# Kernel optimization log

Hardware: AMD Instinct MI355X
Metric: run time of the kernel (lower is better)

The kernel has to match this reference:

```python
import jax, jax.numpy as jnp
import numpy as np

EMB_DIM = 512
NUM_HEADS = 8
SEQ_LEN = 4096
BATCH = 4


def setup_inputs() -> dict:
    key = jax.random.key(0)
    k = jax.random.split(key, 5)
    E = EMB_DIM
    scale = 1.0 / np.sqrt(E)
    x = jax.random.normal(k[0], (BATCH, SEQ_LEN, E), dtype=jnp.float32)
    Wqkv = jax.random.normal(k[1], (E, 3 * E), dtype=jnp.float32) * scale
    bqkv = jax.random.normal(k[2], (3 * E,), dtype=jnp.float32) * 0.01
    Wo = jax.random.normal(k[3], (E, E), dtype=jnp.float32) * scale
    bo = jax.random.normal(k[4], (E,), dtype=jnp.float32) * 0.01
    return {"x": x, "Wqkv": Wqkv, "bqkv": bqkv, "Wo": Wo, "bo": bo}


def reference(x, Wqkv, bqkv, Wo, bo):
    B, S, E = x.shape
    H = NUM_HEADS
    Dh = E // H
    qkv = x @ Wqkv + bqkv                      # [B,S,3E]
    q, k, v = jnp.split(qkv, 3, axis=-1)
    # [B,S,E] -> [B,H,S,Dh]
    q = q.reshape(B, S, H, Dh).transpose(0, 2, 1, 3)
    k = k.reshape(B, S, H, Dh).transpose(0, 2, 1, 3)
    v = v.reshape(B, S, H, Dh).transpose(0, 2, 1, 3)
    att = jnp.einsum("bhsd,bhtd->bhst", q, k) / jnp.sqrt(jnp.asarray(Dh, x.dtype))
    causal = jnp.tril(jnp.ones((S, S), dtype=bool))
    att = jnp.where(causal[None, None], att, -jnp.inf)
    att = jax.nn.softmax(att, axis=-1)
    out = jnp.einsum("bhst,bhtd->bhsd", att, v)  # [B,H,S,Dh]
    out = out.transpose(0, 2, 1, 3).reshape(B, S, E)
    return out @ Wo + bo
```

## Files before the change

kernel.cpp:

```cpp
#include <hip/hip_runtime.h>
#include <math.h>

#define NB 4
#define NS 4096
#define NE 512
#define NH 8
#define ND 64
#define N3 1536
#define NM (NB*NS)

typedef __attribute__((ext_vector_type(8))) short bf16x8;
typedef __attribute__((ext_vector_type(4))) float f32x4;
typedef unsigned short ushort_t;

#define QSCALE 0.18033688011f

extern "C" __device__ float __ocml_native_exp2_f32(float);

__device__ __forceinline__ unsigned int pk2bf(float a, float b) {
    unsigned int r;
    asm("v_cvt_pk_bf16_f32 %0, %1, %2" : "=v"(r) : "v"(a), "v"(b));
    return r;
}

__device__ __forceinline__ unsigned short f2bf(float f) {
    return (unsigned short)(pk2bf(f, f) & 0xFFFFu);
}

typedef __attribute__((address_space(1))) const void g_void;
typedef __attribute__((address_space(3))) void l_void;
__device__ __forceinline__ void cp16(const void* g, void* l) {
    __builtin_amdgcn_global_load_lds((g_void*)g, (l_void*)l, 16, 0, 0);
}

__global__ __launch_bounds__(256)
void cast_x(const float* __restrict__ x, ushort_t* __restrict__ xb) {
    const size_t i = ((size_t)blockIdx.x * 256 + threadIdx.x) * 4;
    float4 v = *(const float4*)&x[i];
    uint2 o;
    o.x = pk2bf(v.x, v.y);
    o.y = pk2bf(v.z, v.w);
    *(uint2*)&xb[i] = o;
}

__global__ __launch_bounds__(256)
void cast_wT(const float* __restrict__ W, ushort_t* __restrict__ WT, int N) {
    __shared__ ushort_t T[64][72];
    const int t = threadIdx.x;
    const int k0 = blockIdx.y * 64, n0 = blockIdx.x * 64;
    const int tx = t & 15, ty = t >> 4;
    #pragma unroll
    for (int p = 0; p < 4; ++p) {
        const int r = p * 16 + ty;
        float4 v = *(const float4*)&W[(size_t)(k0 + r) * N + n0 + tx * 4];
        const unsigned int u01 = pk2bf(v.x, v.y);
        const unsigned int u23 = pk2bf(v.z, v.w);
        T[tx*4+0][r] = (ushort_t)(u01 & 0xFFFFu);
        T[tx*4+1][r] = (ushort_t)(u01 >> 16);
        T[tx*4+2][r] = (ushort_t)(u23 & 0xFFFFu);
        T[tx*4+3][r] = (ushort_t)(u23 >> 16);
    }
    __syncthreads();
    const int nn = t >> 2, kc = (t & 3) * 16;
    uint4 a = *(uint4*)&T[nn][kc];
    uint4 b = *(uint4*)&T[nn][kc + 8];
    *(uint4*)&WT[(size_t)(n0 + nn) * 512 + k0 + kc]     = a;
    *(uint4*)&WT[(size_t)(n0 + nn) * 512 + k0 + kc + 8] = b;
}

__global__ __launch_bounds__(256)
void qkv_mfma(const ushort_t* __restrict__ xb, const ushort_t* __restrict__ WT,
              const float* __restrict__ bqkv,
              ushort_t* __restrict__ Qb, ushort_t* __restrict__ Kb,
              ushort_t* __restrict__ Vb)
{
    __shared__ ushort_t As[128 * 32];
    __shared__ ushort_t Bs[128 * 32];
    const int tid = threadIdx.x;
    const int lane = tid & 63, w = tid >> 6;
    const int col = lane & 15, quad = lane >> 4;
    const int wm = w & 1, wn = w >> 1;
    const int m0 = blockIdx.y * 128;
    const int nblk = blockIdx.x * 128;

    const int arow = tid >> 2, ach = (tid & 3) * 8;
    const ushort_t* aSrc = xb + (size_t)(m0 + arow) * 512 + ach;
    const ushort_t* bSrc = WT + (size_t)(nblk + arow) * 512 + ach;
    ushort_t* aDst = As + tid * 8;
    ushort_t* bDst = Bs + tid * 8;

    f32x4 acc[4][4];
    #pragma unroll
    for (int i = 0; i < 4; ++i)
        #pragma unroll
        for (int j = 0; j < 4; ++j)
            #pragma unroll
            for (int r = 0; r < 4; ++r) acc[i][j][r] = 0.f;

    for (int k0 = 0; k0 < 512; k0 += 32) {
        __syncthreads();
        cp16(aSrc + k0, aDst);
        cp16(aSrc + 64 * 512 + k0, aDst + 2048);
        cp16(bSrc + k0, bDst);
        cp16(bSrc + 64 * 512 + k0, bDst + 2048);
        __syncthreads();
        bf16x8 af[4], bf[4];
        #pragma unroll
        for (int mt = 0; mt < 4; ++mt)
            af[mt] = *(const bf16x8*)&As[(wm*64 + mt*16 + col) * 32 + quad*8];
        #pragma unroll
        for (int nt = 0; nt < 4; ++nt)
            bf[nt] = *(const bf16x8*)&Bs[(wn*64 + nt*16 + col) * 32 + quad*8];
        #pragma unroll
        for (int nt = 0; nt < 4; ++nt)
            #pragma unroll
            for (int mt = 0; mt < 4; ++mt)
                acc[mt][nt] = __builtin_amdgcn_mfma_f32_16x16x32_bf16(
                    af[mt], bf[nt], acc[mt][nt], 0, 0, 0);
    }

    const int which = nblk >> 9;
    const float scale = (which == 0) ? QSCALE : 1.0f;
    const int b = m0 >> 12;
    const int s0 = m0 & (NS - 1);
    float bias[4];
    int hh[4], dd[4];
    #pragma unroll
    for (int nt = 0; nt < 4; ++nt) {
        const int n = nblk + wn*64 + nt*16 + col;
        bias[nt] = bqkv[n];
        const int e = n & (NE - 1);
        hh[nt] = e >> 6; dd[nt] = e & 63;
    }
    if (which == 2) {
        #pragma unroll
        for (int mt = 0; mt < 4; ++mt) {
            const int s = s0 + wm*64 + mt*16 + quad*4;
            #pragma unroll
            for (int nt = 0; nt < 4; ++nt) {
                uint2 pv;
                pv.x = pk2bf(acc[mt][nt][0] + bias[nt],
                             acc[mt][nt][1] + bias[nt]);
                pv.y = pk2bf(acc[mt][nt][2] + bias[nt],
                             acc[mt][nt][3] + bias[nt]);
                *(uint2*)&Vb[((size_t)(b*NH + hh[nt]) * ND + dd[nt]) * NS + s] = pv;
            }
        }
    } else {
        ushort_t* dst = (which == 0) ? Qb : Kb;
        #pragma unroll
        for (int mt = 0; mt < 4; ++mt) {
            const int s = s0 + wm*64 + mt*16 + quad*4;
            #pragma unroll
            for (int nt = 0; nt < 4; ++nt) {
                const unsigned int u01 =
                    pk2bf((acc[mt][nt][0] + bias[nt]) * scale,
                          (acc[mt][nt][1] + bias[nt]) * scale);
                const unsigned int u23 =
                    pk2bf((acc[mt][nt][2] + bias[nt]) * scale,
                          (acc[mt][nt][3] + bias[nt]) * scale);
                const size_t a0 = ((size_t)(b*NH + hh[nt]) * NS + s) * ND + dd[nt];
                dst[a0]          = (ushort_t)(u01 & 0xFFFFu);
                dst[a0 + ND]     = (ushort_t)(u01 >> 16);
                dst[a0 + 2*ND]   = (ushort_t)(u23 & 0xFFFFu);
                dst[a0 + 3*ND]   = (ushort_t)(u23 >> 16);
            }
        }
    }
}

__global__ __launch_bounds__(256)
void flash_mfma(const ushort_t* __restrict__ Qb,
                const ushort_t* __restrict__ Kb,
                const ushort_t* __restrict__ Vb,
                ushort_t* __restrict__ Ob)
{
    __shared__ __align__(16) ushort_t Ks[64][72];
    __shared__ __align__(16) ushort_t VT[64][72];
    __shared__ __align__(16) ushort_t Ps[4][32][72];

    const int tid  = threadIdx.x;
    const int w    = tid >> 6;
    const int lane = tid & 63;
    const int col  = lane & 15;
    const int quad = lane >> 4;
    const int qpair = blockIdx.x;
    const int bh   = blockIdx.y;
    const size_t base = (size_t)bh * NS * ND;

    const int r  = tid & 63;
    const int dg = tid >> 6;
    const ushort_t* kbase = Kb + base + (size_t)r * ND + dg*16;
    const ushort_t* vbase = Vb + base + (size_t)r * NS + dg*16;

    bf16x8 ones;
    {
        const short o = (col == 0) ? (short)0x3F80 : (short)0;
        #pragma unroll
        for (int j = 0; j < 8; ++j) ones[j] = o;
    }

    #pragma unroll 1
    for (int phase = 0; phase < 2; ++phase) {
        const int qv = phase ? (31 - qpair) : qpair;

        bf16x8 aq[2][2];
        #pragma unroll
        for (int mt = 0; mt < 2; ++mt)
            #pragma unroll
            for (int kh = 0; kh < 2; ++kh)
                aq[mt][kh] = *(const bf16x8*)
                    &Qb[base + (size_t)(qv*128 + w*32 + mt*16 + col) * ND
                        + kh*32 + quad*8];

        f32x4 acc[2][4];
        f32x4 lacc[2];
        #pragma unroll
        for (int mt = 0; mt < 2; ++mt) {
            #pragma unroll
            for (int r2 = 0; r2 < 4; ++r2) lacc[mt][r2] = 0.f;
            #pragma unroll
            for (int nt = 0; nt < 4; ++nt)
                #pragma unroll
                for (int r2 = 0; r2 < 4; ++r2) acc[mt][nt][r2] = 0.f;
        }

        const int nkt = 2 * qv + 2;

        uint4 kr0, kr1, vr0, vr1;
        {
            const ushort_t* ks = kbase;
            kr0 = *(const uint4*)ks;
            kr1 = *(const uint4*)(ks + 8);
            const ushort_t* vs = vbase;
            vr0 = *(const uint4*)vs;
            vr1 = *(const uint4*)(vs + 8);
        }

        for (int kt = 0; kt < nkt; ++kt) {
            __syncthreads();
            *(uint4*)&Ks[r][dg*16]     = kr0;
            *(uint4*)&Ks[r][dg*16 + 8] = kr1;
            *(uint4*)&VT[r][dg*16]     = vr0;
            *(uint4*)&VT[r][dg*16 + 8] = vr1;
            __syncthreads();

            if (kt + 1 < nkt) {
                const ushort_t* ks = kbase + (size_t)(kt+1) * 64 * ND;
                kr0 = *(const uint4*)ks;
                kr1 = *(const uint4*)(ks + 8);
                const ushort_t* vs = vbase + (kt+1) * 64;
                vr0 = *(const uint4*)vs;
                vr1 = *(const uint4*)(vs + 8);
            }

            if (kt*64 >= qv*128 + w*32 + 32) continue;

            f32x4 s[2][4];
            #pragma unroll
            for (int mt = 0; mt < 2; ++mt)
                #pragma unroll
                for (int nt = 0; nt < 4; ++nt)
                    #pragma unroll
                    for (int r2 = 0; r2 < 4; ++r2) s[mt][nt][r2] = 0.f;

            #pragma unroll
            for (int nt = 0; nt < 4; ++nt)
                #pragma unroll
                for (int kh = 0; kh < 2; ++kh) {
                    bf16x8 ak = *(const bf16x8*)&Ks[nt*16 + col][kh*32 + quad*8];
                    #pragma unroll
                    for (int mt = 0; mt < 2; ++mt)
                        s[mt][nt] = __builtin_amdgcn_mfma_f32_16x16x32_bf16(
                            ak, aq[mt][kh], s[mt][nt], 0, 0, 0);
                }

            if (kt >= 2 * qv) {
                #pragma unroll
                for (int mt = 0; mt < 2; ++mt) {
                    const int qrow = qv*128 + w*32 + mt*16 + col;
                    #pragma unroll
                    for (int nt = 0; nt < 4; ++nt) {
                        const int key = kt*64 + nt*16 + quad*4;
                        #pragma unroll
                        for (int reg = 0; reg < 4; ++reg)
                            if (key + reg > qrow) s[mt][nt][reg] = -1e30f;
                    }
                }
            }

            #pragma unroll
            for (int mt = 0; mt < 2; ++mt)
                #pragma unroll
                for (int nt = 0; nt < 4; ++nt) {
                    uint2 pw;
                    pw.x = pk2bf(__ocml_native_exp2_f32(s[mt][nt][0]),
                                 __ocml_native_exp2_f32(s[mt][nt][1]));
                    pw.y = pk2bf(__ocml_native_exp2_f32(s[mt][nt][2]),
                                 __ocml_native_exp2_f32(s[mt][nt][3]));
                    *(uint2*)&Ps[w][mt*16 + col][nt*16 + quad*4] = pw;
                }

            bf16x8 ap[2][2];
            #pragma unroll
            for (int mt = 0; mt < 2; ++mt)
                #pragma unroll
                for (int kh = 0; kh < 2; ++kh)
                    ap[mt][kh] = *(const bf16x8*)&Ps[w][mt*16 + col][kh*32 + quad*8];

            #pragma unroll
            for (int mt = 0; mt < 2; ++mt)
                #pragma unroll
                for (int kh = 0; kh < 2; ++kh)
                    lacc[mt] = __builtin_amdgcn_mfma_f32_16x16x32_bf16(
                        ap[mt][kh], ones, lacc[mt], 0, 0, 0);

            #pragma unroll
            for (int nt = 0; nt < 4; ++nt)
                #pragma unroll
                for (int kh = 0; kh < 2; ++kh) {
                    bf16x8 bv = *(const bf16x8*)&VT[nt*16 + col][kh*32 + quad*8];
                    #pragma unroll
                    for (int mt = 0; mt < 2; ++mt)
                        acc[mt][nt] = __builtin_amdgcn_mfma_f32_16x16x32_bf16(
                            ap[mt][kh], bv, acc[mt][nt], 0, 0, 0);
                }
        }

        #pragma unroll
        for (int mt = 0; mt < 2; ++mt)
            #pragma unroll
            for (int reg = 0; reg < 4; ++reg) {
                const float l = __shfl(lacc[mt][reg], lane & 48, 64);
                const float inv = 1.f / l;
                const int row = qv*128 + w*32 + mt*16 + quad*4 + reg;
                const unsigned int u01 = pk2bf(acc[0 + (mt<<0)][0][reg] * 0.f +
                                               acc[mt][0][reg] * inv,
                                               acc[mt][1][reg] * inv);
                const unsigned int u23 = pk2bf(acc[mt][2][reg] * inv,
                                               acc[mt][3][reg] * inv);
                ushort_t* op = &Ob[base + (size_t)row * ND + col];
                op[0]  = (ushort_t)(u01 & 0xFFFFu);
                op[16] = (ushort_t)(u01 >> 16);
                op[32] = (ushort_t)(u23 & 0xFFFFu);
                op[48] = (ushort_t)(u23 >> 16);
            }
    }
}

__global__ __launch_bounds__(256)
void out_mfma(const ushort_t* __restrict__ Ob, const ushort_t* __restrict__ WT,
              const float* __restrict__ bo, float* __restrict__ out)
{
    __shared__ ushort_t As[128 * 32];
    __shared__ ushort_t Bs[128 * 32];
    const int tid = threadIdx.x;
    const int lane = tid & 63, w = tid >> 6;
    const int col = lane & 15, quad = lane >> 4;
    const int wm = w & 1, wn = w >> 1;
    const int m0 = blockIdx.y * 128;
    const int nblk = blockIdx.x * 128;

    const int arow = tid >> 2, ach = (tid & 3) * 8;
    const int bblk = m0 >> 12;
    const int s0 = m0 & (NS - 1);
    const ushort_t* bSrc = WT + (size_t)(nblk + arow) * 512 + ach;
    ushort_t* aDst = As + tid * 8;
    ushort_t* bDst = Bs + tid * 8;

    f32x4 acc[4][4];
    #pragma unroll
    for (int i = 0; i < 4; ++i)
        #pragma unroll
        for (int j = 0; j < 4; ++j)
            #pragma unroll
            for (int r = 0; r < 4; ++r) acc[i][j][r] = 0.f;

    for (int k0 = 0; k0 < 512; k0 += 32) {
        __syncthreads();
        const int h = k0 >> 6, koff = k0 & 63;
        const ushort_t* aS =
            Ob + ((size_t)(bblk*NH + h) * NS + s0 + arow) * ND + koff + ach;
        cp16(aS, aDst);
        cp16(aS + 64 * ND, aDst + 2048);
        cp16(bSrc + k0, bDst);
        cp16(bSrc + 64 * 512 + k0, bDst + 2048);
        __syncthreads();
        bf16x8 af[4], bf[4];
        #pragma unroll
        for (int mt = 0; mt < 4; ++mt)
            af[mt] = *(const bf16x8*)&As[(wm*64 + mt*16 + col) * 32 + quad*8];
        #pragma unroll
        for (int nt = 0; nt < 4; ++nt)
            bf[nt] = *(const bf16x8*)&Bs[(wn*64 + nt*16 + col) * 32 + quad*8];
        #pragma unroll
        for (int nt = 0; nt < 4; ++nt)
            #pragma unroll
            for (int mt = 0; mt < 4; ++mt)
                acc[mt][nt] = __builtin_amdgcn_mfma_f32_16x16x32_bf16(
                    af[mt], bf[nt], acc[mt][nt], 0, 0, 0);
    }

    float bias[4];
    #pragma unroll
    for (int nt = 0; nt < 4; ++nt)
        bias[nt] = bo[nblk + wn*64 + nt*16 + col];
    #pragma unroll
    for (int mt = 0; mt < 4; ++mt)
        #pragma unroll
        for (int reg = 0; reg < 4; ++reg) {
            const int m = m0 + wm*64 + mt*16 + quad*4 + reg;
            #pragma unroll
            for (int nt = 0; nt < 4; ++nt)
                out[(size_t)m * NE + nblk + wn*64 + nt*16 + col] =
                    acc[mt][nt][reg] + bias[nt];
        }
}

extern "C" void kernel_launch(void* const* d_in, const int* in_sizes, int n_in,
                              void* d_out, int out_size, void* d_ws, size_t ws_size,
                              hipStream_t stream) {
    const float* x    = (const float*)d_in[0];
    const float* Wqkv = (const float*)d_in[1];
    const float* bqkv = (const float*)d_in[2];
    const float* Wo   = (const float*)d_in[3];
    const float* bo   = (const float*)d_in[4];
    float* out = (float*)d_out;

    const size_t per = (size_t)NB * NH * NS * ND;
    ushort_t* ws = (ushort_t*)d_ws;
    ushort_t* xb     = ws;
    ushort_t* Ob     = ws;
    ushort_t* Qb     = ws + per;
    ushort_t* Kb     = Qb + per;
    ushort_t* Vb     = Kb + per;
    ushort_t* WqkvT  = Vb + per;
    ushort_t* WoT    = WqkvT + (size_t)N3 * NE;

    dim3 blk(256);
    cast_x<<<dim3(NM * NE / 1024), blk, 0, stream>>>(x, xb);
    cast_wT<<<dim3(N3/64, NE/64), blk, 0, stream>>>(Wqkv, WqkvT, N3);
    cast_wT<<<dim3(NE/64, NE/64), blk, 0, stream>>>(Wo, WoT, NE);
    qkv_mfma<<<dim3(N3/128, NM/128), blk, 0, stream>>>(xb, WqkvT, bqkv, Qb, Kb, Vb);
    flash_mfma<<<dim3(16, NB*NH), blk, 0, stream>>>(Qb, Kb, Vb, Ob);
    out_mfma<<<dim3(NE/128, NM/128), blk, 0, stream>>>(Ob, WoT, bo, out);
}
```

Measured before the change: 256.7 us.

## Split flash attention block into 8 waves of 16 query rows each

The flash attention kernel now launches 512 threads per block with 8 waves, each owning 16 query rows instead of 32. The K/V tile staging is split across the 8 waves at 8 elements per thread, and each wave keeps its own P tile in shared memory. The aim is more waves per block to hide latency and finer causal skipping per wave. In exchange each wave does half the MFMA work per K/V tile load, so there is more synchronisation and LDS traffic per unit of compute.

```diff
diff --git a/kernel.cpp b/kernel.cpp
--- a/kernel.cpp
+++ b/kernel.cpp
@@ -169,7 +169,7 @@
     }
 }
 
-__global__ __launch_bounds__(256)
+__global__ __launch_bounds__(512)
 void flash_mfma(const ushort_t* __restrict__ Qb,
                 const ushort_t* __restrict__ Kb,
                 const ushort_t* __restrict__ Vb,
@@ -177,7 +177,7 @@
 {
     __shared__ __align__(16) ushort_t Ks[64][72];
     __shared__ __align__(16) ushort_t VT[64][72];
-    __shared__ __align__(16) ushort_t Ps[4][32][72];
+    __shared__ __align__(16) ushort_t Ps[8][16][72];
 
     const int tid  = threadIdx.x;
     const int w    = tid >> 6;
@@ -190,8 +190,8 @@
 
     const int r  = tid & 63;
     const int dg = tid >> 6;
-    const ushort_t* kbase = Kb + base + (size_t)r * ND + dg*16;
-    const ushort_t* vbase = Vb + base + (size_t)r * NS + dg*16;
+    const ushort_t* kbase = Kb + base + (size_t)r * ND + dg*8;
+    const ushort_t* vbase = Vb + base + (size_t)r * NS + dg*8;
 
     bf16x8 ones;
     {
@@ -204,147 +204,109 @@
     for (int phase = 0; phase < 2; ++phase) {
         const int qv = phase ? (31 - qpair) : qpair;
 
-        bf16x8 aq[2][2];
-        #pragma unroll
-        for (int mt = 0; mt < 2; ++mt)
-            #pragma unroll
-            for (int kh = 0; kh < 2; ++kh)
-                aq[mt][kh] = *(const bf16x8*)
-                    &Qb[base + (size_t)(qv*128 + w*32 + mt*16 + col) * ND
-                        + kh*32 + quad*8];
-
-        f32x4 acc[2][4];
-        f32x4 lacc[2];
-        #pragma unroll
-        for (int mt = 0; mt < 2; ++mt) {
-            #pragma unroll
-            for (int r2 = 0; r2 < 4; ++r2) lacc[mt][r2] = 0.f;
+        bf16x8 aq[2];
+        #pragma unroll
+        for (int kh = 0; kh < 2; ++kh)
+            aq[kh] = *(const bf16x8*)
+                &Qb[base + (size_t)(qv*128 + w*16 + col) * ND + kh*32 + quad*8];
+
+        f32x4 acc[4];
+        f32x4 lacc;
+        #pragma unroll
+        for (int r2 = 0; r2 < 4; ++r2) lacc[r2] = 0.f;
+        #pragma unroll
+        for (int nt = 0; nt < 4; ++nt)
+            #pragma unroll
+            for (int r2 = 0; r2 < 4; ++r2) acc[nt][r2] = 0.f;
+
+        const int nkt = 2 * qv + 2;
+
+        uint4 kr, vr;
+        kr = *(const uint4*)kbase;
+        vr = *(const uint4*)vbase;
+
+        for (int kt = 0; kt < nkt; ++kt) {
+            __syncthreads();
+            *(uint4*)&Ks[r][dg*8] = kr;
+            *(uint4*)&VT[r][dg*8] = vr;
+            __syncthreads();
+
+            if (kt + 1 < nkt) {
+                kr = *(const uint4*)(kbase + (size_t)(kt+1) * 64 * ND);
+                vr = *(const uint4*)(vbase + (kt+1) * 64);
+            }
+
+            if (kt*64 >= qv*128 + w*16 + 16) continue;
+
+            f32x4 s[4];
             #pragma unroll
             for (int nt = 0; nt < 4; ++nt)
                 #pragma unroll
-                for (int r2 = 0; r2 < 4; ++r2) acc[mt][nt][r2] = 0.f;
-        }
-
-        const int nkt = 2 * qv + 2;
-
-        uint4 kr0, kr1, vr0, vr1;
-        {
-            const ushort_t* ks = kbase;
-            kr0 = *(const uint4*)ks;
-            kr1 = *(const uint4*)(ks + 8);
-            const ushort_t* vs = vbase;
-            vr0 = *(const uint4*)vs;
-            vr1 = *(const uint4*)(vs + 8);
-        }
-
-        for (int kt = 0; kt < nkt; ++kt) {
-            __syncthreads();
-            *(uint4*)&Ks[r][dg*16]     = kr0;
-            *(uint4*)&Ks[r][dg*16 + 8] = kr1;
-            *(uint4*)&VT[r][dg*16]     = vr0;
-            *(uint4*)&VT[r][dg*16 + 8] = vr1;
-            __syncthreads();
-
-            if (kt + 1 < nkt) {
-                const ushort_t* ks = kbase + (size_t)(kt+1) * 64 * ND;
-                kr0 = *(const uint4*)ks;
-                kr1 = *(const uint4*)(ks + 8);
-                const ushort_t* vs = vbase + (kt+1) * 64;
-                vr0 = *(const uint4*)vs;
-                vr1 = *(const uint4*)(vs + 8);
-            }
-
-            if (kt*64 >= qv*128 + w*32 + 32) continue;
-
-            f32x4 s[2][4];
-            #pragma unroll
-            for (int mt = 0; mt < 2; ++mt)
-                #pragma unroll
-                for (int nt = 0; nt < 4; ++nt)
-                    #pragma unroll
-                    for (int r2 = 0; r2 < 4; ++r2) s[mt][nt][r2] = 0.f;
+                for (int r2 = 0; r2 < 4; ++r2) s[nt][r2] = 0.f;
 
             #pragma unroll
             for (int nt = 0; nt < 4; ++nt)
                 #pragma unroll
                 for (int kh = 0; kh < 2; ++kh) {
                     bf16x8 ak = *(const bf16x8*)&Ks[nt*16 + col][kh*32 + quad*8];
+                    s[nt] = __builtin_amdgcn_mfma_f32_16x16x32_bf16(
+                        ak, aq[kh], s[nt], 0, 0, 0);
+                }
+
+            if (kt >= 2 * qv) {
+                const int qrow = qv*128 + w*16 + col;
+                #pragma unroll
+                for (int nt = 0; nt < 4; ++nt) {
+                    const int key = kt*64 + nt*16 + quad*4;
                     #pragma unroll
-                    for (int mt = 0; mt < 2; ++mt)
-                        s[mt][nt] = __builtin_amdgcn_mfma_f32_16x16x32_bf16(
-                            ak, aq[mt][kh], s[mt][nt], 0, 0, 0);
-                }
-
-            if (kt >= 2 * qv) {
-                #pragma unroll
-                for (int mt = 0; mt < 2; ++mt) {
-                    const int qrow = qv*128 + w*32 + mt*16 + col;
-                    #pragma unroll
-                    for (int nt = 0; nt < 4; ++nt) {
-                        const int key = kt*64 + nt*16 + quad*4;
-                        #pragma unroll
-                        for (int reg = 0; reg < 4; ++reg)
-                            if (key + reg > qrow) s[mt][nt][reg] = -1e30f;
-                    }
+                    for (int reg = 0; reg < 4; ++reg)
+                        if (key + reg > qrow) s[nt][reg] = -1e30f;
                 }
             }
 
             #pragma unroll
-            for (int mt = 0; mt < 2; ++mt)
-                #pragma unroll
-                for (int nt = 0; nt < 4; ++nt) {
-                    uint2 pw;
-                    pw.x = pk2bf(__ocml_native_exp2_f32(s[mt][nt][0]),
-                                 __ocml_native_exp2_f32(s[mt][nt][1]));
-                    pw.y = pk2bf(__ocml_native_exp2_f32(s[mt][nt][2]),
-                                 __ocml_native_exp2_f32(s[mt][nt][3]));
-                    *(uint2*)&Ps[w][mt*16 + col][nt*16 + quad*4] = pw;
-                }
-
-            bf16x8 ap[2][2];
-            #pragma unroll
-            for (int mt = 0; mt < 2; ++mt)
-                #pragma unroll
-                for (int kh = 0; kh < 2; ++kh)
-                    ap[mt][kh] = *(const bf16x8*)&Ps[w][mt*16 + col][kh*32 + quad*8];
-
-            #pragma unroll
-            for (int mt = 0; mt < 2; ++mt)
-                #pragma unroll
-                for (int kh = 0; kh < 2; ++kh)
-                    lacc[mt] = __builtin_amdgcn_mfma_f32_16x16x32_bf16(
-                        ap[mt][kh], ones, lacc[mt], 0, 0, 0);
+            for (int nt = 0; nt < 4; ++nt) {
+                uint2 pw;
+                pw.x = pk2bf(__ocml_native_exp2_f32(s[nt][0]),
+                             __ocml_native_exp2_f32(s[nt][1]));
+                pw.y = pk2bf(__ocml_native_exp2_f32(s[nt][2]),
+                             __ocml_native_exp2_f32(s[nt][3]));
+                *(uint2*)&Ps[w][col][nt*16 + quad*4] = pw;
+            }
+
+            bf16x8 ap[2];
+            #pragma unroll
+            for (int kh = 0; kh < 2; ++kh)
+                ap[kh] = *(const bf16x8*)&Ps[w][col][kh*32 + quad*8];
+
+            #pragma unroll
+            for (int kh = 0; kh < 2; ++kh)
+                lacc = __builtin_amdgcn_mfma_f32_16x16x32_bf16(
+                    ap[kh], ones, lacc, 0, 0, 0);
 
             #pragma unroll
             for (int nt = 0; nt < 4; ++nt)
                 #pragma unroll
                 for (int kh = 0; kh < 2; ++kh) {
                     bf16x8 bv = *(const bf16x8*)&VT[nt*16 + col][kh*32 + quad*8];
-                    #pragma unroll
-                    for (int mt = 0; mt < 2; ++mt)
-                        acc[mt][nt] = __builtin_amdgcn_mfma_f32_16x16x32_bf16(
-                            ap[mt][kh], bv, acc[mt][nt], 0, 0, 0);
+                    acc[nt] = __builtin_amdgcn_mfma_f32_16x16x32_bf16(
+                        ap[kh], bv, acc[nt], 0, 0, 0);
                 }
         }
 
         #pragma unroll
-        for (int mt = 0; mt < 2; ++mt)
-            #pragma unroll
-            for (int reg = 0; reg < 4; ++reg) {
-                const float l = __shfl(lacc[mt][reg], lane & 48, 64);
-                const float inv = 1.f / l;
-                const int row = qv*128 + w*32 + mt*16 + quad*4 + reg;
-                const unsigned int u01 = pk2bf(acc[0 + (mt<<0)][0][reg] * 0.f +
-                                               acc[mt][0][reg] * inv,
-                                               acc[mt][1][reg] * inv);
-                const unsigned int u23 = pk2bf(acc[mt][2][reg] * inv,
-                                               acc[mt][3][reg] * inv);
-                ushort_t* op = &Ob[base + (size_t)row * ND + col];
-                op[0]  = (ushort_t)(u01 & 0xFFFFu);
-                op[16] = (ushort_t)(u01 >> 16);
-                op[32] = (ushort_t)(u23 & 0xFFFFu);
-                op[48] = (ushort_t)(u23 >> 16);
-            }
+        for (int reg = 0; reg < 4; ++reg) {
+            const float l = __shfl(lacc[reg], lane & 48, 64);
+            const float inv = 1.f / l;
+            const int row = qv*128 + w*16 + quad*4 + reg;
+            const unsigned int u01 = pk2bf(acc[0][reg] * inv, acc[1][reg] * inv);
+            const unsigned int u23 = pk2bf(acc[2][reg] * inv, acc[3][reg] * inv);
+            ushort_t* op = &Ob[base + (size_t)row * ND + col];
+            op[0]  = (ushort_t)(u01 & 0xFFFFu);
+            op[16] = (ushort_t)(u01 >> 16);
+            op[32] = (ushort_t)(u23 & 0xFFFFu);
+            op[48] = (ushort_t)(u23 >> 16);
+        }
     }
 }
 
@@ -442,6 +404,6 @@
     cast_wT<<<dim3(N3/64, NE/64), blk, 0, stream>>>(Wqkv, WqkvT, N3);
     cast_wT<<<dim3(NE/64, NE/64), blk, 0, stream>>>(Wo, WoT, NE);
     qkv_mfma<<<dim3(N3/128, NM/128), blk, 0, stream>>>(xb, WqkvT, bqkv, Qb, Kb, Vb);
-    flash_mfma<<<dim3(16, NB*NH), blk, 0, stream>>>(Qb, Kb, Vb, Ob);
+    flash_mfma<<<dim3(16, NB*NH), dim3(512), 0, stream>>>(Qb, Kb, Vb, Ob);
     out_mfma<<<dim3(NE/128, NM/128), blk, 0, stream>>>(Ob, WoT, bo, out);
 }
```

Result: no change. 260.2 us (+1.4%).
